# Kernel optimization log

Measured on AMD Instinct MI355X. Metric: run time of the kernel, lower is better.

## Reference

```python
import jax, jax.numpy as jnp
import numpy as np

N = 4_000_000   # points at level d
SIDE = 1024     # coordinate range per axis
HALF = SIDE // 2  # parent coord range


def setup_inputs() -> dict:
    key = jax.random.key(0)
    k1, k2 = jax.random.split(key)
    xyz = jax.random.randint(k1, (N, 3), 0, SIDE, dtype=jnp.int32)
    b = (jnp.arange(N, dtype=jnp.int32) % 4)[:, None]  # 4 batches
    coords = jnp.concatenate([b, xyz], axis=1)          # (N,4): [b,x,y,z]
    kernel = jnp.ones((8,), dtype=jnp.float32)          # frozen all-ones 2x2x2 conv weights
    return {"coords": coords, "kernel": kernel}


def _fog(coords, kernel):
    # pos(): occupancy code 2**(x%2 + 2*y%2 + 4*z%2)
    bits = coords[:, 1:4] & 1                       # (N,3)
    off = bits[:, 0] + 2 * bits[:, 1] + 4 * bits[:, 2]  # (N,) child offset in 2x2x2 window
    pos = jnp.exp2(off.astype(jnp.float32))         # (N,) code in {1,2,4,...,128}
    contrib = pos * kernel[off]                     # per-offset conv weight (all ones)
    # stride-2 conv: parent voxel = floor(xyz/2); linearize (b,z,y,x) into a key
    parent = coords[:, 1:4] >> 1                    # (N,3)
    keys = (((coords[:, 0].astype(jnp.int64) * HALF + parent[:, 2]) * HALF
             + parent[:, 1]) * HALF + parent[:, 0])
    ukeys, inv = jnp.unique(keys, return_inverse=True, size=N, fill_value=-1)
    feats = jax.ops.segment_sum(contrib, inv, num_segments=N)[:, None]  # (N,1)
    # decode padded unique keys back to coords; pad slots -> -1
    px = (ukeys % HALF).astype(jnp.int32)
    py = ((ukeys // HALF) % HALF).astype(jnp.int32)
    pz = ((ukeys // (HALF * HALF)) % HALF).astype(jnp.int32)
    pb = (ukeys // (HALF * HALF * HALF)).astype(jnp.int32)
    valid = (ukeys >= 0)[:, None]
    coords_out = jnp.where(valid, jnp.stack([pb, px, py, pz], axis=1), -1)
    return coords_out, feats


def reference(coords, kernel):
    return _fog(coords, kernel)
```

## Files before the change

### kernel.cpp

```cpp
#include <hip/hip_runtime.h>
#include <stdint.h>

typedef unsigned int u32;
typedef unsigned long long u64;

#define LBITS  14
#define LMASK  ((1u << LBITS) - 1u)
#define NBUCK  (1u << (29 - LBITS))
#define BWORDS (1u << (LBITS - 5))
#define WPL    (BWORDS / 64)
#define WOPAD  (BWORDS + BWORDS / 32)
#define FCAP   224
#define BPB    4
#define TILE_A 4096
#define RPT    (TILE_A / 256)
#define CCAP   16384
#define P2T    1024
#define RPT2U  (CCAP / P2T)

__device__ __forceinline__ u32 woidx(u32 w) { return w + (w >> 5); }

__device__ __forceinline__ void wsync() {
    asm volatile("s_waitcnt lgkmcnt(0)" ::: "memory");
}

__device__ __forceinline__ u32 make_key(int4 c) {
    return ((((u32)c.x * 512u + ((u32)c.w >> 1)) * 512u + ((u32)c.z >> 1)) * 512u)
           + ((u32)c.y >> 1);
}

__global__ void zero1(u32* __restrict__ p, u32 g) {
    u32 i = blockIdx.x * 256u + threadIdx.x;
    if (i < g) p[i] = 0u;
}

__global__ void __launch_bounds__(256) part1f(const int4* __restrict__ coords,
        u32* __restrict__ ccur, u32* __restrict__ tmp, int n) {
    __shared__ u32 stage[TILE_A];
    __shared__ u32 hcnt[256];
    __shared__ u32 eb[256];
    __shared__ u32 gb[256];
    __shared__ u32 wtot[4];
    u32 t = threadIdx.x, wave = t >> 6, lane = t & 63u;
    u32 base = blockIdx.x * TILE_A;
    u32 m = min((u32)TILE_A, (u32)n - base);
    hcnt[t] = 0u;
    __syncthreads();
    u32 recv[RPT]; u32 seqv[RPT];
    #pragma unroll
    for (int k = 0; k < RPT; ++k) {
        u32 j = (u32)k * 256u + t;
        if (j < m) {
            int4 c = coords[base + j];
            u32 key = make_key(c);
            u32 off = ((u32)c.y & 1u) | (((u32)c.z & 1u) << 1) | (((u32)c.w & 1u) << 2);
            u32 rec = (key << 3) | off;
            recv[k] = rec;
            seqv[k] = atomicAdd(&hcnt[rec >> 24], 1u);
        }
    }
    __syncthreads();
    u32 v = hcnt[t];
    u32 incl = v;
    #pragma unroll
    for (int d = 1; d < 64; d <<= 1) {
        u32 x = __shfl_up(incl, d);
        if ((int)lane >= d) incl += x;
    }
    if (lane == 63u) wtot[wave] = incl;
    __syncthreads();
    u32 off = (wave > 0u ? wtot[0] : 0u) + (wave > 1u ? wtot[1] : 0u)
            + (wave > 2u ? wtot[2] : 0u);
    u32 excl = off + incl - v;
    u32 gbase = atomicAdd(&ccur[t * 16u], v);
    eb[t] = excl;
    gb[t] = (t << 14) + gbase - excl;
    __syncthreads();
    #pragma unroll
    for (int k = 0; k < RPT; ++k) {
        u32 j = (u32)k * 256u + t;
        if (j < m) {
            u32 rec = recv[k];
            stage[eb[rec >> 24] + seqv[k]] = rec;
        }
    }
    __syncthreads();
    for (u32 j = t; j < m; j += 256u) {
        u32 rec = stage[j];
        tmp[gb[rec >> 24] + j] = rec;
    }
}

__global__ void __launch_bounds__(P2T) part2u(u32* __restrict__ tmp,
        const u32* __restrict__ ccur, u32* __restrict__ cstart,
        u32* __restrict__ bcnt, u32* __restrict__ ucnt,
        u32* __restrict__ lexc, u32* __restrict__ utot) {
    __shared__ u32 stage[CCAP];
    __shared__ u32 h[128];
    __shared__ u32 lstart[128];
    __shared__ u32 cnts[128];
    __shared__ u32 ucl[128];
    __shared__ u32 wtot[2];
    __shared__ u32 bm[16][WOPAD];
    __shared__ u32 Wt[16][BWORDS];
    u32 t = threadIdx.x, wave = t >> 6, lane = t & 63u;
    u32 c = blockIdx.x;
    u32 base = c << 14;
    u32 L = ccur[c * 16u];
    if (t < 128u) h[t] = 0u;
    __syncthreads();
    u32 recv[RPT2U];
    #pragma unroll
    for (int k = 0; k < RPT2U; ++k) {
        u32 j = (u32)k * P2T + t;
        if (j < L) {
            u32 rec = tmp[base + j];
            u32 sq = atomicAdd(&h[(rec >> 17) & 127u], 1u);
            recv[k] = (sq << 24) | (rec & 0xFFFFFFu);
        }
    }
    __syncthreads();
    u32 v = 0, incl = 0;
    if (t < 128u) {
        v = h[t];
        incl = v;
        #pragma unroll
        for (int d = 1; d < 64; d <<= 1) {
            u32 x = __shfl_up(incl, d);
            if ((int)lane >= d) incl += x;
        }
        if (lane == 63u) wtot[t >> 6] = incl;
    }
    __syncthreads();
    if (t < 128u) {
        u32 off = (t >= 64u) ? wtot[0] : 0u;
        u32 excl = off + incl - v;
        lstart[t] = excl;
        cnts[t] = v;
        u32 bucket = (c << 7) | t;
        cstart[bucket] = base + excl;
        bcnt[bucket] = v;
    }
    __syncthreads();
    #pragma unroll
    for (int k = 0; k < RPT2U; ++k) {
        u32 j = (u32)k * P2T + t;
        if (j < L) {
            u32 pr = recv[k];
            stage[lstart[(pr >> 17) & 127u] + (pr >> 24)] = pr & 0x1FFFFu;
        }
    }
    __syncthreads();
    u32* B = bm[wave];
    u32* W = Wt[wave];
    for (u32 bi = 0; bi < 8u; ++bi) {
        u32 b = wave * 8u + bi;
        #pragma unroll
        for (int j = 0; j < WPL; ++j) B[woidx(lane * WPL + j)] = 0u;
        wsync();
        u32 s0 = lstart[b], cnt = cnts[b];
        for (u32 i = s0 + lane; i < s0 + cnt; i += 64u) {
            u32 lk = (stage[i] >> 3) & LMASK;
            atomicOr(&B[woidx(lk >> 5)], 1u << (lk & 31u));
        }
        wsync();
        u32 pc[WPL]; u32 sum = 0;
        #pragma unroll
        for (int j = 0; j < WPL; ++j) { pc[j] = __popc(B[woidx(lane * WPL + j)]); sum += pc[j]; }
        u32 inc2 = sum;
        #pragma unroll
        for (int d = 1; d < 64; d <<= 1) {
            u32 x = __shfl_up(inc2, d);
            if ((int)lane >= d) inc2 += x;
        }
        u32 lex = inc2 - sum;
        {
            u32 r = lex;
            #pragma unroll
            for (int j = 0; j < WPL; ++j) { W[((u32)j << 6) | lane] = r; r += pc[j]; }
        }
        if (lane == 63u) ucl[b] = inc2;
        wsync();
        for (u32 i = s0 + lane; i < s0 + cnt; i += 64u) {
            u32 rec = stage[i];
            u32 lk = (rec >> 3) & LMASK;
            u32 w = lk >> 5, bit = lk & 31u;
            u32 r = W[((w & 7u) << 6) | (w >> 3)]
                  + __popc(B[woidx(w)] & ((1u << bit) - 1u));
            stage[i] = (r << 17) | (rec & 0x1FFFFu);
        }
        wsync();
    }
    __syncthreads();
    for (u32 j = t; j < L; j += P2T) tmp[base + j] = stage[j];
    if (t < 128u) ucnt[(c << 7) | t] = ucl[t];
    __syncthreads();
    u32 uv = 0, incl2 = 0;
    if (t < 128u) {
        uv = ucl[t];
        incl2 = uv;
        #pragma unroll
        for (int d = 1; d < 64; d <<= 1) {
            u32 x = __shfl_up(incl2, d);
            if ((int)lane >= d) incl2 += x;
        }
        if (lane == 63u) wtot[t >> 6] = incl2;
    }
    __syncthreads();
    if (t < 128u) {
        u32 off = (t >= 64u) ? wtot[0] : 0u;
        lexc[(c << 7) | t] = off + incl2 - uv;
        if (t == 127u) utot[c] = wtot[0] + incl2;
    }
}

__global__ void __launch_bounds__(256) pass_emit(const u32* __restrict__ buckrec,
        const u32* __restrict__ cstart, const u32* __restrict__ bcnt,
        const u32* __restrict__ ucnt, const u32* __restrict__ lexc,
        const u32* __restrict__ utot, const float* __restrict__ kern,
        float4* __restrict__ rows, float* __restrict__ feats, int n) {
    __shared__ float fl[BPB][FCAP];
    __shared__ u32 kl[BPB][FCAP];
    __shared__ float ksc[BPB][8];
    u32 wave = threadIdx.x >> 6, lane = threadIdx.x & 63u;
    u32 bucket = blockIdx.x * BPB + wave;
    float* F = fl[wave];
    u32* K = kl[wave];
    #pragma unroll
    for (u32 j = lane; j < FCAP; j += 64u) F[j] = 0.f;
    if (lane < 8u) ksc[wave][lane] = (float)(1u << lane) * kern[lane];
    wsync();
    u32 start = cstart[bucket];
    u32 cnt = bcnt[bucket];
    u32 uc = ucnt[bucket];
    u32 c = bucket >> 7;
    u32 cb = 0, Uall = 0;
    #pragma unroll
    for (int k = 0; k < 4; ++k) {
        u32 j = (u32)k * 64u + lane;
        u32 uv = utot[j];
        Uall += uv;
        cb += (j < c) ? uv : 0u;
    }
    #pragma unroll
    for (int d = 1; d < 64; d <<= 1) {
        cb += __shfl_xor(cb, d);
        Uall += __shfl_xor(Uall, d);
    }
    u32 base = cb + lexc[bucket];
    for (u32 i = start + lane; i < start + cnt; i += 64u) {
        u32 rec = buckrec[i];
        u32 r = rec >> 17;
        atomicAdd(&F[r], ksc[wave][rec & 7u]);
        K[r] = (rec >> 3) & LMASK;
    }
    wsync();
    u32 keyhi = bucket << LBITS;
    for (u32 j = lane; j < uc; j += 64u) {
        u32 key = keyhi | K[j];
        rows[base + j] = make_float4((float)(key >> 27), (float)(key & 511u),
                                     (float)((key >> 9) & 511u),
                                     (float)((key >> 18) & 511u));
        feats[base + j] = F[j];
    }
    u32 len = (u32)n - Uall;
    u32 per = (len + (u32)NBUCK - 1u) / (u32)NBUCK;
    u32 ps = Uall + bucket * per;
    u32 pe = min(ps + per, (u32)n);
    for (u32 i = ps + lane; i < pe; i += 64u) {
        rows[i] = make_float4(-1.f, -1.f, -1.f, -1.f);
        feats[i] = 0.f;
    }
}

extern "C" void kernel_launch(void* const* d_in, const int* in_sizes, int n_in,
                              void* d_out, int out_size, void* d_ws, size_t ws_size,
                              hipStream_t stream) {
    const int n = in_sizes[0] / 4;
    const int4* coords = (const int4*)d_in[0];
    const float* kern  = (const float*)d_in[1];
    const u32 NT = ((u32)n + TILE_A - 1) / TILE_A;

    u32* wsp = (u32*)d_ws;
    u32* tmp     = wsp;
    u32* ccur    = tmp + 256 * CCAP;
    u32* cstart  = ccur + 256 * 16;
    u32* bcnt    = cstart + NBUCK;
    u32* ucnt    = bcnt + NBUCK;
    u32* lexc    = ucnt + NBUCK;
    u32* utot    = lexc + NBUCK;

    float4* rows  = (float4*)d_out;
    float*  feats = (float*)((char*)d_out + (size_t)n * 16);

    zero1<<<16, 256, 0, stream>>>(ccur, 256 * 16);
    part1f<<<NT, 256, 0, stream>>>(coords, ccur, tmp, n);
    part2u<<<256, P2T, 0, stream>>>(tmp, ccur, cstart, bcnt, ucnt, lexc, utot);
    pass_emit<<<NBUCK / BPB, 256, 0, stream>>>(tmp, cstart, bcnt, ucnt, lexc, utot,
                                               kern, rows, feats, n);
}
```

Measured before the change: 191.6 us.

## Split each coarse partition across two part2u blocks by half-buckets

```diff
diff --git a/kernel.cpp b/kernel.cpp
--- a/kernel.cpp
+++ b/kernel.cpp
@@ -14,9 +14,10 @@
 #define BPB    4
 #define TILE_A 4096
 #define RPT    (TILE_A / 256)
-#define CCAP   16384
+#define CCAP   17408
+#define HCAP   8704
 #define P2T    1024
-#define RPT2U  (CCAP / P2T)
+#define RPT2U  ((CCAP + P2T - 1) / P2T)
 
 __device__ __forceinline__ u32 woidx(u32 w) { return w + (w >> 5); }
 
@@ -74,7 +75,7 @@
     u32 excl = off + incl - v;
     u32 gbase = atomicAdd(&ccur[t * 16u], v);
     eb[t] = excl;
-    gb[t] = (t << 14) + gbase - excl;
+    gb[t] = t * (u32)CCAP + gbase - excl;
     __syncthreads();
     #pragma unroll
     for (int k = 0; k < RPT; ++k) {
@@ -94,67 +95,65 @@
 __global__ void __launch_bounds__(P2T) part2u(u32* __restrict__ tmp,
         const u32* __restrict__ ccur, u32* __restrict__ cstart,
         u32* __restrict__ bcnt, u32* __restrict__ ucnt,
-        u32* __restrict__ lexc, u32* __restrict__ utot) {
-    __shared__ u32 stage[CCAP];
-    __shared__ u32 h[128];
-    __shared__ u32 lstart[128];
-    __shared__ u32 cnts[128];
-    __shared__ u32 ucl[128];
-    __shared__ u32 wtot[2];
+        u32* __restrict__ lexc, u32* __restrict__ htot) {
+    __shared__ u32 stage[HCAP];
+    __shared__ u32 sh_h[64];
+    __shared__ u32 lstart[64];
+    __shared__ u32 cnts[64];
+    __shared__ u32 ucl[64];
+    __shared__ u32 shLh[1];
     __shared__ u32 bm[16][WOPAD];
-    __shared__ u32 Wt[16][BWORDS];
+    __shared__ u32 wof8[16][64];
     u32 t = threadIdx.x, wave = t >> 6, lane = t & 63u;
-    u32 c = blockIdx.x;
-    u32 base = c << 14;
+    u32 c = blockIdx.x >> 1, h = blockIdx.x & 1u;
+    u32 base = c * (u32)CCAP;
+    u32 hbase = base + h * (u32)HCAP;
     u32 L = ccur[c * 16u];
-    if (t < 128u) h[t] = 0u;
+    if (t < 64u) sh_h[t] = 0u;
     __syncthreads();
     u32 recv[RPT2U];
     #pragma unroll
     for (int k = 0; k < RPT2U; ++k) {
         u32 j = (u32)k * P2T + t;
+        recv[k] = 0xFFFFFFFFu;
         if (j < L) {
             u32 rec = tmp[base + j];
-            u32 sq = atomicAdd(&h[(rec >> 17) & 127u], 1u);
-            recv[k] = (sq << 24) | (rec & 0xFFFFFFu);
-        }
-    }
-    __syncthreads();
-    u32 v = 0, incl = 0;
-    if (t < 128u) {
-        v = h[t];
-        incl = v;
+            if (((rec >> 23) & 1u) == h) {
+                u32 sq = atomicAdd(&sh_h[(rec >> 17) & 63u], 1u);
+                recv[k] = (sq << 24) | (rec & 0xFFFFFFu);
+            }
+        }
+    }
+    __syncthreads();
+    if (t < 64u) {
+        u32 v = sh_h[t];
+        u32 incl = v;
         #pragma unroll
         for (int d = 1; d < 64; d <<= 1) {
             u32 x = __shfl_up(incl, d);
             if ((int)lane >= d) incl += x;
         }
-        if (lane == 63u) wtot[t >> 6] = incl;
-    }
-    __syncthreads();
-    if (t < 128u) {
-        u32 off = (t >= 64u) ? wtot[0] : 0u;
-        u32 excl = off + incl - v;
+        u32 excl = incl - v;
         lstart[t] = excl;
         cnts[t] = v;
-        u32 bucket = (c << 7) | t;
-        cstart[bucket] = base + excl;
+        u32 bucket = (c << 7) | (h << 6) | t;
+        cstart[bucket] = hbase + excl;
         bcnt[bucket] = v;
-    }
-    __syncthreads();
+        if (t == 63u) shLh[0] = incl;
+    }
+    __syncthreads();
+    u32 Lh = shLh[0];
     #pragma unroll
     for (int k = 0; k < RPT2U; ++k) {
-        u32 j = (u32)k * P2T + t;
-        if (j < L) {
-            u32 pr = recv[k];
-            stage[lstart[(pr >> 17) & 127u] + (pr >> 24)] = pr & 0x1FFFFu;
-        }
+        u32 pr = recv[k];
+        if (pr != 0xFFFFFFFFu)
+            stage[lstart[(pr >> 17) & 63u] + (pr >> 24)] = pr & 0x1FFFFu;
     }
     __syncthreads();
     u32* B = bm[wave];
-    u32* W = Wt[wave];
-    for (u32 bi = 0; bi < 8u; ++bi) {
-        u32 b = wave * 8u + bi;
+    u32* W8 = wof8[wave];
+    for (u32 bi = 0; bi < 4u; ++bi) {
+        u32 b = wave * 4u + bi;
         #pragma unroll
         for (int j = 0; j < WPL; ++j) B[woidx(lane * WPL + j)] = 0u;
         wsync();
@@ -164,60 +163,51 @@
             atomicOr(&B[woidx(lk >> 5)], 1u << (lk & 31u));
         }
         wsync();
-        u32 pc[WPL]; u32 sum = 0;
-        #pragma unroll
-        for (int j = 0; j < WPL; ++j) { pc[j] = __popc(B[woidx(lane * WPL + j)]); sum += pc[j]; }
+        u32 sum = 0;
+        #pragma unroll
+        for (int j = 0; j < WPL; ++j) sum += __popc(B[woidx(lane * WPL + j)]);
         u32 inc2 = sum;
         #pragma unroll
         for (int d = 1; d < 64; d <<= 1) {
             u32 x = __shfl_up(inc2, d);
             if ((int)lane >= d) inc2 += x;
         }
-        u32 lex = inc2 - sum;
-        {
-            u32 r = lex;
-            #pragma unroll
-            for (int j = 0; j < WPL; ++j) { W[((u32)j << 6) | lane] = r; r += pc[j]; }
-        }
+        W8[lane] = inc2 - sum;
         if (lane == 63u) ucl[b] = inc2;
         wsync();
         for (u32 i = s0 + lane; i < s0 + cnt; i += 64u) {
             u32 rec = stage[i];
             u32 lk = (rec >> 3) & LMASK;
             u32 w = lk >> 5, bit = lk & 31u;
-            u32 r = W[((w & 7u) << 6) | (w >> 3)]
-                  + __popc(B[woidx(w)] & ((1u << bit) - 1u));
+            u32 g = w >> 3;
+            u32 r = W8[g];
+            for (u32 k = g * 8u; k < w; ++k) r += __popc(B[woidx(k)]);
+            r += __popc(B[woidx(w)] & ((1u << bit) - 1u));
             stage[i] = (r << 17) | (rec & 0x1FFFFu);
         }
         wsync();
     }
     __syncthreads();
-    for (u32 j = t; j < L; j += P2T) tmp[base + j] = stage[j];
-    if (t < 128u) ucnt[(c << 7) | t] = ucl[t];
-    __syncthreads();
-    u32 uv = 0, incl2 = 0;
-    if (t < 128u) {
-        uv = ucl[t];
-        incl2 = uv;
+    for (u32 j = t; j < Lh; j += P2T) tmp[hbase + j] = stage[j];
+    if (t < 64u) ucnt[(c << 7) | (h << 6) | t] = ucl[t];
+    __syncthreads();
+    if (t < 64u) {
+        u32 uv = ucl[t];
+        u32 incl2 = uv;
         #pragma unroll
         for (int d = 1; d < 64; d <<= 1) {
             u32 x = __shfl_up(incl2, d);
             if ((int)lane >= d) incl2 += x;
         }
-        if (lane == 63u) wtot[t >> 6] = incl2;
-    }
-    __syncthreads();
-    if (t < 128u) {
-        u32 off = (t >= 64u) ? wtot[0] : 0u;
-        lexc[(c << 7) | t] = off + incl2 - uv;
-        if (t == 127u) utot[c] = wtot[0] + incl2;
+        lexc[(c << 7) | (h << 6) | t] = incl2 - uv;
+        if (t == 63u) htot[(c << 1) | h] = incl2;
     }
 }
 
 __global__ void __launch_bounds__(256) pass_emit(const u32* __restrict__ buckrec,
         const u32* __restrict__ cstart, const u32* __restrict__ bcnt,
         const u32* __restrict__ ucnt, const u32* __restrict__ lexc,
-        const u32* __restrict__ utot, const float* __restrict__ kern,
+        const u32* __restrict__ htot, const float* __restrict__ kern,
         float4* __restrict__ rows, float* __restrict__ feats, int n) {
     __shared__ float fl[BPB][FCAP];
     __shared__ u32 kl[BPB][FCAP];
@@ -233,14 +223,14 @@
     u32 start = cstart[bucket];
     u32 cnt = bcnt[bucket];
     u32 uc = ucnt[bucket];
-    u32 c = bucket >> 7;
+    u32 ch = bucket >> 6;
     u32 cb = 0, Uall = 0;
     #pragma unroll
-    for (int k = 0; k < 4; ++k) {
+    for (int k = 0; k < 8; ++k) {
         u32 j = (u32)k * 64u + lane;
-        u32 uv = utot[j];
+        u32 uv = htot[j];
         Uall += uv;
-        cb += (j < c) ? uv : 0u;
+        cb += (j < ch) ? uv : 0u;
     }
     #pragma unroll
     for (int d = 1; d < 64; d <<= 1) {
@@ -288,14 +278,14 @@
     u32* bcnt    = cstart + NBUCK;
     u32* ucnt    = bcnt + NBUCK;
     u32* lexc    = ucnt + NBUCK;
-    u32* utot    = lexc + NBUCK;
+    u32* htot    = lexc + NBUCK;
 
     float4* rows  = (float4*)d_out;
     float*  feats = (float*)((char*)d_out + (size_t)n * 16);
 
     zero1<<<16, 256, 0, stream>>>(ccur, 256 * 16);
     part1f<<<NT, 256, 0, stream>>>(coords, ccur, tmp, n);
-    part2u<<<256, P2T, 0, stream>>>(tmp, ccur, cstart, bcnt, ucnt, lexc, utot);
-    pass_emit<<<NBUCK / BPB, 256, 0, stream>>>(tmp, cstart, bcnt, ucnt, lexc, utot,
+    part2u<<<512, P2T, 0, stream>>>(tmp, ccur, cstart, bcnt, ucnt, lexc, htot);
+    pass_emit<<<NBUCK / BPB, 256, 0, stream>>>(tmp, cstart, bcnt, ucnt, lexc, htot,
                                                kern, rows, feats, n);
 }
```

Result: slower. 202.6 us (+5.7%).
